# Kernel optimization log

Hardware: AMD Instinct MI355X
Metric: run time of the kernel (lower is better)

## Reference

```python
import jax, jax.numpy as jnp
import numpy as np

N = 100000
E = 1600000
D_IN = 128
D_OUT = 128

def setup_inputs() -> dict:
    key = jax.random.key(0)
    k1, k2, k3, k4, k5, k6 = jax.random.split(key, 6)
    h = jax.random.normal(k1, (N, D_IN), dtype=jnp.float32)
    # norm ~ deg^{-1/2}; use positive uniform values as stand-in
    norm = jax.random.uniform(k2, (N, 1), dtype=jnp.float32, minval=0.05, maxval=1.0)
    src = jax.random.randint(k3, (E,), 0, N, dtype=jnp.int32)
    dst = jax.random.randint(k4, (E,), 0, N, dtype=jnp.int32)
    weight = jax.random.normal(k5, (D_IN, D_OUT), dtype=jnp.float32) * (2.0 / (D_IN + D_OUT)) ** 0.5
    bias = jnp.zeros((D_OUT,), dtype=jnp.float32)
    return {"h": h, "norm": norm, "src": src, "dst": dst, "weight": weight, "bias": bias}

def reference(h, norm, src, dst, weight, bias):
    n_nodes = h.shape[0]
    hw = h @ weight                      # [N, D_out] dense GEMM
    hw = hw * norm                       # pre-aggregation degree scale
    msgs = hw[src]                       # gather: [E, D_out]
    agg = jax.ops.segment_sum(msgs, dst, num_segments=n_nodes)  # scatter-sum
    out = agg * norm + bias              # post-scale + bias
    return out
```

## Files before the change

kernel.cpp:

```cpp
#include <hip/hip_runtime.h>
#include <hip/hip_bf16.h>
#include <hip/hip_cooperative_groups.h>

namespace cg = cooperative_groups;

#define D 128
#define D4 32
#define CHUNK 6400
#define KSLOT 7
#define MAXB 2048
#define NSEG 8
#define SL 4096

typedef __attribute__((ext_vector_type(8))) short bf16x8;
typedef __attribute__((ext_vector_type(8))) unsigned short ushort8;
typedef __attribute__((ext_vector_type(4))) float f32x4;

static __device__ __forceinline__ float bf2f(unsigned short u) {
    return __uint_as_float(((unsigned)u) << 16);
}
static __device__ __forceinline__ unsigned pk2(float x, float y) {
    float2 f; f.x = x; f.y = y;
    __hip_bfloat162 b = __float22bfloat162_rn(f);
    return *(unsigned*)&b;
}

__global__ __launch_bounds__(256) void wcvt_kernel(
    const float* __restrict__ W, unsigned short* __restrict__ Wt)
{
    const int idx = blockIdx.x * 256 + threadIdx.x;
    const float4 w = ((const float4*)W)[idx];
    const int k = idx >> 5;
    const int c = (idx & 31) * 4;
    const unsigned q01 = pk2(w.x, w.y);
    const unsigned q23 = pk2(w.z, w.w);
    Wt[(c + 0) * 128 + k] = (unsigned short)(q01 & 0xFFFFu);
    Wt[(c + 1) * 128 + k] = (unsigned short)(q01 >> 16);
    Wt[(c + 2) * 128 + k] = (unsigned short)(q23 & 0xFFFFu);
    Wt[(c + 3) * 128 + k] = (unsigned short)(q23 >> 16);
}

__global__ __launch_bounds__(512) void gemm_mfma_kernel(
    const float* __restrict__ h, const unsigned short* __restrict__ Wt,
    const float* __restrict__ norm, unsigned short* __restrict__ hwb,
    int n_nodes)
{
    __shared__ unsigned short Bs[128 * 136];

    const int t = threadIdx.x;
    const int row0 = blockIdx.x * 128;

    #pragma unroll
    for (int i = 0; i < 4; ++i) {
        const int idx = t + 512 * i;
        const int c = idx >> 4;
        const int k8 = idx & 15;
        *(ushort8*)&Bs[c * 136 + k8 * 8] = ((const ushort8*)Wt)[idx];
    }
    __syncthreads();

    const int wv = t >> 6;
    const int lane = t & 63;
    const int m = lane & 15;
    const int quad = lane >> 4;

    long gra = row0 + wv * 16 + m;
    if (gra >= n_nodes) gra = n_nodes - 1;
    const float* hrow = h + gra * D;

    f32x4 acc[8];
    #pragma unroll
    for (int nt = 0; nt < 8; ++nt) { f32x4 z = {0.f, 0.f, 0.f, 0.f}; acc[nt] = z; }

    #pragma unroll
    for (int kt = 0; kt < 4; ++kt) {
        const float4 a0 = *(const float4*)(hrow + kt * 32 + quad * 8);
        const float4 a1 = *(const float4*)(hrow + kt * 32 + quad * 8 + 4);
        bf16x8 af;
        unsigned* aw = (unsigned*)&af;
        aw[0] = pk2(a0.x, a0.y);
        aw[1] = pk2(a0.z, a0.w);
        aw[2] = pk2(a1.x, a1.y);
        aw[3] = pk2(a1.z, a1.w);
        #pragma unroll
        for (int nt = 0; nt < 8; ++nt) {
            const bf16x8 bfr = *(const bf16x8*)&Bs[(nt * 16 + m) * 136 + kt * 32 + quad * 8];
            acc[nt] = __builtin_amdgcn_mfma_f32_16x16x32_bf16(af, bfr, acc[nt], 0, 0, 0);
        }
    }

    float nv[4];
    #pragma unroll
    for (int i = 0; i < 4; ++i) {
        const int gr = row0 + wv * 16 + quad * 4 + i;
        nv[i] = (gr < n_nodes) ? norm[gr] : 0.f;
    }

    __syncthreads();
    #pragma unroll
    for (int nt = 0; nt < 8; ++nt) {
        const unsigned q01 = pk2(acc[nt][0] * nv[0], acc[nt][1] * nv[1]);
        const unsigned q23 = pk2(acc[nt][2] * nv[2], acc[nt][3] * nv[3]);
        const int rb = wv * 16 + quad * 4;
        Bs[(rb + 0) * 136 + nt * 16 + m] = (unsigned short)(q01 & 0xFFFFu);
        Bs[(rb + 1) * 136 + nt * 16 + m] = (unsigned short)(q01 >> 16);
        Bs[(rb + 2) * 136 + nt * 16 + m] = (unsigned short)(q23 & 0xFFFFu);
        Bs[(rb + 3) * 136 + nt * 16 + m] = (unsigned short)(q23 >> 16);
    }
    __syncthreads();

    #pragma unroll
    for (int i2 = 0; i2 < 4; ++i2) {
        const int idx = t + 512 * i2;
        const int r = idx >> 4;
        const int c8 = idx & 15;
        const int gr = row0 + r;
        if (gr < n_nodes)
            *(ushort8*)&hwb[(size_t)gr * D + c8 * 8] =
                *(const ushort8*)&Bs[r * 136 + c8 * 8];
    }
}

__global__ __launch_bounds__(1024) void coop_edge_kernel(
    const int* __restrict__ src, const int* __restrict__ dst,
    int* __restrict__ H, int* __restrict__ PS, int* __restrict__ SB,
    int* __restrict__ boff,
    unsigned int* __restrict__ ebuf, int* __restrict__ srcs_g,
    const unsigned short* __restrict__ hwb,
    const float* __restrict__ norm, const float* __restrict__ bias,
    float* __restrict__ out,
    int n_edges, int n_nodes, int EB, int NBUCK)
{
    __shared__ int smem[SL + 192];

    cg::grid_group grid = cg::this_grid();
    const int t = threadIdx.x;
    const int g = blockIdx.x;
    const int gid = g * 1024 + t;
    const int glen = (EB + NSEG - 1) / NSEG;
    const int e0 = g * CHUNK;
    const int e1 = min(e0 + CHUNK, n_edges);

    int ed[KSLOT], es[KSLOT], er[KSLOT];
    {
        int* lbh = smem;
        for (int i = t; i < MAXB; i += 1024) lbh[i] = 0;
        if (g == 0 && t < 32) {
            ushort4 z; z.x = z.y = z.z = z.w = 0;
            ((ushort4*)(hwb + (size_t)n_nodes * D))[t] = z;
        }
        __syncthreads();
        #pragma unroll
        for (int k = 0; k < KSLOT; ++k) {
            const int e = e0 + t + 1024 * k;
            if (e < e1) {
                ed[k] = dst[e];
                es[k] = src[e];
                er[k] = atomicAdd(&lbh[ed[k] >> 6], 1);
            } else { ed[k] = -1; es[k] = 0; er[k] = 0; }
        }
        __syncthreads();
        for (int i = t; i < MAXB; i += 1024) H[(size_t)g * MAXB + i] = lbh[i];
    }
    grid.sync();

    if (gid < NSEG * MAXB) {
        const int seg = gid >> 11;
        const int c = gid & (MAXB - 1);
        const int g0 = seg * glen, g1 = min(g0 + glen, EB);
        int s = 0;
        for (int gg = g0; gg < g1; ++gg) s += H[(size_t)gg * MAXB + c];
        PS[seg * MAXB + c] = s;
    }
    grid.sync();

    if (g == 0) {
        int* tmp = smem;
        const int cA = 2 * t, cB = 2 * t + 1;
        int va = 0, vb = 0;
        #pragma unroll
        for (int sg = 0; sg < NSEG; ++sg) { va += PS[sg * MAXB + cA]; vb += PS[sg * MAXB + cB]; }
        tmp[t] = va + vb;
        __syncthreads();
        for (int ofs = 1; ofs < 1024; ofs <<= 1) {
            const int x = (t >= ofs) ? tmp[t - ofs] : 0;
            __syncthreads();
            tmp[t] += x;
            __syncthreads();
        }
        const int run = tmp[t] - (va + vb);
        boff[cA] = run;
        boff[cB] = run + va;
        if (t == 1023) boff[MAXB] = tmp[1023];
        int sb = run;
        #pragma unroll
        for (int sg = 0; sg < NSEG; ++sg) { SB[sg * MAXB + cA] = sb; sb += PS[sg * MAXB + cA]; }
        sb = run + va;
        #pragma unroll
        for (int sg = 0; sg < NSEG; ++sg) { SB[sg * MAXB + cB] = sb; sb += PS[sg * MAXB + cB]; }
    }
    grid.sync();

    {
        int* lofs = smem;
        const int seg = g / glen;
        const int g0s = seg * glen;
        for (int i = t; i < MAXB; i += 1024) {
            int run = SB[seg * MAXB + i];
            for (int gg = g0s; gg < g; ++gg) run += H[(size_t)gg * MAXB + i];
            lofs[i] = run;
        }
        __syncthreads();
        #pragma unroll
        for (int k = 0; k < KSLOT; ++k) {
            if (ed[k] >= 0)
                ebuf[lofs[ed[k] >> 6] + er[k]] =
                    (unsigned)es[k] | ((unsigned)(ed[k] & 63) << 17);
        }
    }
    grid.sync();

    {
        int* slds = smem;
        int* lcnt = smem + SL;
        int* lcur = smem + SL + 64;
        int* loff = smem + SL + 128;
        const ushort4* hw4 = (const ushort4*)hwb;
        const int grp = t >> 5;
        const int l = t & 31;
        const float4 bs = ((const float4*)bias)[l];

        for (int bkt = g; bkt < NBUCK; bkt += gridDim.x) {
            __syncthreads();
            if (t < 64) lcnt[t] = 0;
            __syncthreads();
            const int w0 = boff[bkt], w1 = boff[bkt + 1];
            const int wlen = w1 - w0;
            const bool uselds = (wlen + 480) <= SL;
            const int gbase = w0 + 448 * bkt;
            const int gn0 = bkt * 64;

            unsigned rc[4];
            if (uselds) {
                #pragma unroll
                for (int k = 0; k < 4; ++k) {
                    const int e = w0 + t + k * 1024;
                    if (e < w1) {
                        rc[k] = ebuf[e];
                        atomicAdd(&lcnt[(rc[k] >> 17) & 63], 1);
                    }
                }
            } else {
                for (int e = w0 + t; e < w1; e += 1024)
                    atomicAdd(&lcnt[(ebuf[e] >> 17) & 63], 1);
            }
            __syncthreads();
            if (t < 64) {
                const int c = lcnt[t];
                const int p = (c + 7) & ~7;
                int x = p;
                #pragma unroll
                for (int ofs = 1; ofs < 64; ofs <<= 1) {
                    const int y = __shfl_up(x, ofs, 64);
                    if (t >= ofs) x += y;
                }
                const int base = x - p;
                lcur[t] = base;
                loff[t] = base;
            }
            __syncthreads();
            if (uselds) {
                #pragma unroll
                for (int k = 0; k < 4; ++k) {
                    const int e = w0 + t + k * 1024;
                    if (e < w1) {
                        const unsigned rec = rc[k];
                        const int loc = (rec >> 17) & 63;
                        const int pos = atomicAdd(&lcur[loc], 1);
                        slds[pos] = (int)(rec & 0x1FFFFu);
                    }
                }
            } else {
                for (int e = w0 + t; e < w1; e += 1024) {
                    const unsigned rec = ebuf[e];
                    const int loc = (rec >> 17) & 63;
                    const int pos = atomicAdd(&lcur[loc], 1);
                    srcs_g[gbase + pos] = (int)(rec & 0x1FFFFu);
                }
            }
            for (int w = t; w < 512; w += 1024) {
                const int ln = w >> 3, k = w & 7;
                const int gn = gn0 + ln;
                if (gn < n_nodes) {
                    const int c = lcnt[ln];
                    const int pad = (8 - (c & 7)) & 7;
                    if (k < pad) {
                        const int pos = loff[ln] + c + k;
                        if (uselds) slds[pos] = n_nodes; else srcs_g[gbase + pos] = n_nodes;
                    }
                }
            }
            __syncthreads();

            #pragma unroll
            for (int nn = 0; nn < 2; ++nn) {
                const int loc = grp * 2 + nn;
                const int gn = gn0 + loc;
                if (gn >= n_nodes) continue;
                const int start = loff[loc];
                const int deg = lcnt[loc];
                const int nb8 = (deg + 7) >> 3;
                float4 acc; acc.x = acc.y = acc.z = acc.w = 0.f;
                int myidx = 0;
                for (int bb = 0; bb < nb8; ++bb) {
                    const int q = bb & 3;
                    if (q == 0) {
                        const int ri = start + bb * 8 + l;
                        myidx = uselds ? slds[ri] : srcs_g[gbase + ri];
                    }
                    ushort4 v[8];
                    #pragma unroll
                    for (int jj = 0; jj < 8; ++jj) {
                        const int s = __shfl(myidx, q * 8 + jj, 32);
                        v[jj] = hw4[(long)s * D4 + l];
                    }
                    #pragma unroll
                    for (int jj = 0; jj < 8; ++jj) {
                        acc.x += bf2f(v[jj].x);
                        acc.y += bf2f(v[jj].y);
                        acc.z += bf2f(v[jj].z);
                        acc.w += bf2f(v[jj].w);
                    }
                }
                const float nv = norm[gn];
                float4 o;
                o.x = acc.x * nv + bs.x;
                o.y = acc.y * nv + bs.y;
                o.z = acc.z * nv + bs.z;
                o.w = acc.w * nv + bs.w;
                ((float4*)out)[(long)gn * D4 + l] = o;
            }
        }
    }
}

__global__ __launch_bounds__(1024) void hist_kernel(
    const int* __restrict__ dst, int* __restrict__ H,
    unsigned short* __restrict__ hwb, int n_edges, int n_nodes)
{
    __shared__ int lbh[MAXB];
    const int t = threadIdx.x;
    const int g = blockIdx.x;
    for (int i = t; i < MAXB; i += 1024) lbh[i] = 0;
    if (g == 0 && t < 32) {
        ushort4 z; z.x = z.y = z.z = z.w = 0;
        ((ushort4*)(hwb + (size_t)n_nodes * D))[t] = z;
    }
    __syncthreads();
    const int e0 = g * CHUNK;
    const int e1 = min(e0 + CHUNK, n_edges);
    for (int e = e0 + t; e < e1; e += 1024) {
        atomicAdd(&lbh[dst[e] >> 6], 1);
    }
    __syncthreads();
    for (int i = t; i < MAXB; i += 1024) {
        H[(size_t)g * MAXB + i] = lbh[i];
    }
}

__global__ __launch_bounds__(256) void chunkscan_local_kernel(
    const int* __restrict__ H, int* __restrict__ CO, int* __restrict__ PS,
    int eb)
{
    const int b = blockIdx.x * 256 + threadIdx.x;
    const int seg = blockIdx.y;
    const int glen = (eb + NSEG - 1) / NSEG;
    const int g0 = seg * glen;
    const int g1 = min(g0 + glen, eb);
    int run = 0;
    for (int g = g0; g < g1; ++g) {
        CO[(size_t)g * MAXB + b] = run;
        run += H[(size_t)g * MAXB + b];
    }
    PS[seg * MAXB + b] = run;
}

__global__ __launch_bounds__(256) void bucket_scan_kernel(
    const int* __restrict__ PS, int* __restrict__ boff, int* __restrict__ SB)
{
    __shared__ int tmp[256];
    const int t = threadIdx.x;
    int v[8];
    int s = 0;
    #pragma unroll
    for (int k = 0; k < 8; ++k) {
        const int i = t * 8 + k;
        int c = 0;
        #pragma unroll
        for (int sg = 0; sg < NSEG; ++sg) c += PS[sg * MAXB + i];
        v[k] = c; s += c;
    }
    tmp[t] = s;
    __syncthreads();
    for (int ofs = 1; ofs < 256; ofs <<= 1) {
        int x = (t >= ofs) ? tmp[t - ofs] : 0;
        __syncthreads();
        tmp[t] += x;
        __syncthreads();
    }
    int run = tmp[t] - s;
    #pragma unroll
    for (int k = 0; k < 8; ++k) {
        const int i = t * 8 + k;
        boff[i] = run;
        int sb = run;
        #pragma unroll
        for (int sg = 0; sg < NSEG; ++sg) {
            SB[sg * MAXB + i] = sb;
            sb += PS[sg * MAXB + i];
        }
        run += v[k];
    }
    if (t == 255) boff[MAXB] = run;
}

__global__ __launch_bounds__(1024) void bscatter_kernel(
    const int* __restrict__ src, const int* __restrict__ dst,
    const int* __restrict__ CO, const int* __restrict__ SB,
    unsigned int* __restrict__ ebuf, int n_edges, int eb)
{
    __shared__ int lbh[MAXB];
    __shared__ int lofs[MAXB];
    const int t = threadIdx.x;
    const int g = blockIdx.x;
    const int glen = (eb + NSEG - 1) / NSEG;
    const int seg = g / glen;
    for (int i = t; i < MAXB; i += 1024) {
        lbh[i] = 0;
        lofs[i] = SB[seg * MAXB + i] + CO[(size_t)g * MAXB + i];
    }
    __syncthreads();
    const int e0 = g * CHUNK;
    const int e1 = min(e0 + CHUNK, n_edges);
    for (int e = e0 + t; e < e1; e += 1024) {
        const int d = dst[e];
        const int bk = d >> 6;
        const int r = atomicAdd(&lbh[bk], 1);
        ebuf[lofs[bk] + r] = (unsigned)src[e] | ((unsigned)(d & 63) << 17);
    }
}

__global__ __launch_bounds__(256) void fillagg_kernel(
    const unsigned int* __restrict__ ebuf, const int* __restrict__ boff,
    int* __restrict__ srcs_g, const unsigned short* __restrict__ hwb,
    const float* __restrict__ norm, const float* __restrict__ bias,
    float* __restrict__ out, int n_nodes)
{
    __shared__ int slds[SL];
    __shared__ int lcnt[64];
    __shared__ int lcur[64];
    __shared__ int loff[64];
    const int t = threadIdx.x;
    const int b = blockIdx.x;
    const int gn0 = b * 64;

    if (t < 64) lcnt[t] = 0;
    __syncthreads();
    const int w0 = boff[b], w1 = boff[b + 1];
    const int wlen = w1 - w0;
    const bool uselds = (wlen + 480) <= SL;
    const int gbase = w0 + 448 * b;

    for (int e = w0 + t; e < w1; e += 256) {
        atomicAdd(&lcnt[(ebuf[e] >> 17) & 63], 1);
    }
    __syncthreads();
    if (t < 64) {
        const int c = lcnt[t];
        const int p = (c + 7) & ~7;
        int x = p;
        #pragma unroll
        for (int ofs = 1; ofs < 64; ofs <<= 1) {
            const int y = __shfl_up(x, ofs, 64);
            if (t >= ofs) x += y;
        }
        const int base = x - p;
        lcur[t] = base;
        loff[t] = base;
    }
    __syncthreads();
    for (int e = w0 + t; e < w1; e += 256) {
        const unsigned rec = ebuf[e];
        const int loc = (rec >> 17) & 63;
        const int pos = atomicAdd(&lcur[loc], 1);
        const int sv = (int)(rec & 0x1FFFFu);
        if (uselds) slds[pos] = sv; else srcs_g[gbase + pos] = sv;
    }
    for (int w = t; w < 512; w += 256) {
        const int ln = w >> 3, k = w & 7;
        const int gn = gn0 + ln;
        if (gn < n_nodes) {
            const int c = lcnt[ln];
            const int pad = (8 - (c & 7)) & 7;
            if (k < pad) {
                const int pos = loff[ln] + c + k;
                if (uselds) slds[pos] = n_nodes; else srcs_g[gbase + pos] = n_nodes;
            }
        }
    }
    __syncthreads();

    const ushort4* hw4 = (const ushort4*)hwb;
    const int grp = t >> 5;
    const int l = t & 31;
    const float4 bs = ((const float4*)bias)[l];
    for (int nn = 0; nn < 8; ++nn) {
        const int loc = grp * 8 + nn;
        const int gn = gn0 + loc;
        if (gn >= n_nodes) continue;
        const int start = loff[loc];
        const int deg = lcnt[loc];
        const int nb8 = (deg + 7) >> 3;
        float4 acc; acc.x = acc.y = acc.z = acc.w = 0.f;
        int myidx = 0;
        for (int bb = 0; bb < nb8; ++bb) {
            const int q = bb & 3;
            if (q == 0) {
                const int ri = start + bb * 8 + l;
                myidx = uselds ? slds[ri] : srcs_g[gbase + ri];
            }
            ushort4 v[8];
            #pragma unroll
            for (int jj = 0; jj < 8; ++jj) {
                const int s = __shfl(myidx, q * 8 + jj, 32);
                v[jj] = hw4[(long)s * D4 + l];
            }
            #pragma unroll
            for (int jj = 0; jj < 8; ++jj) {
                acc.x += bf2f(v[jj].x);
                acc.y += bf2f(v[jj].y);
                acc.z += bf2f(v[jj].z);
                acc.w += bf2f(v[jj].w);
            }
        }
        const float nv = norm[gn];
        float4 o;
        o.x = acc.x * nv + bs.x;
        o.y = acc.y * nv + bs.y;
        o.z = acc.z * nv + bs.z;
        o.w = acc.w * nv + bs.w;
        ((float4*)out)[(long)gn * D4 + l] = o;
    }
}

__global__ __launch_bounds__(256) void scatter_kernel(
    const unsigned short* __restrict__ hwb, const int* __restrict__ src,
    const int* __restrict__ dst, float* __restrict__ out, int n_edges)
{
    const int idx = blockIdx.x * 256 + threadIdx.x;
    if (idx >= n_edges * D4) return;
    const int e = idx >> 5;
    const int g = idx & 31;
    const int s = src[e];
    const int d = dst[e];
    const ushort4 v = ((const ushort4*)hwb)[(long)s * D4 + g];
    float* o = out + (long)d * D + g * 4;
    atomicAdd(o + 0, bf2f(v.x));
    atomicAdd(o + 1, bf2f(v.y));
    atomicAdd(o + 2, bf2f(v.z));
    atomicAdd(o + 3, bf2f(v.w));
}

__global__ __launch_bounds__(256) void finalize_kernel(
    float* __restrict__ out, const float* __restrict__ norm,
    const float* __restrict__ bias, int n_nodes)
{
    const int idx = blockIdx.x * 256 + threadIdx.x;
    if (idx >= n_nodes * D4) return;
    const int n = idx >> 5;
    const int g = idx & 31;
    float4 v = ((float4*)out)[idx];
    const float nv = norm[n];
    const float4 b = ((const float4*)bias)[g];
    v.x = v.x * nv + b.x;
    v.y = v.y * nv + b.y;
    v.z = v.z * nv + b.z;
    v.w = v.w * nv + b.w;
    ((float4*)out)[idx] = v;
}

extern "C" void kernel_launch(void* const* d_in, const int* in_sizes, int n_in,
                              void* d_out, int out_size, void* d_ws, size_t ws_size,
                              hipStream_t stream) {
    const float* h    = (const float*)d_in[0];
    const float* norm = (const float*)d_in[1];
    const int*   src  = (const int*)d_in[2];
    const int*   dst  = (const int*)d_in[3];
    const float* W    = (const float*)d_in[4];
    const float* bias = (const float*)d_in[5];
    float* out = (float*)d_out;

    const int n_nodes = in_sizes[1];
    const int n_edges = in_sizes[2];

    const int NBUCK = (n_nodes + 63) >> 6;
    const int EB    = (n_edges + CHUNK - 1) / CHUNK;
    const int srcs_len = n_edges + 448 * NBUCK + 64;

    size_t p = 0;
    auto take = [&](size_t bytes) {
        size_t cur = p;
        p += (bytes + 255) & ~(size_t)255;
        return cur;
    };
    const size_t hwb_off  = take(((size_t)n_nodes + 1) * D * sizeof(unsigned short));
    const size_t wt_off   = take((size_t)D * D * sizeof(unsigned short));
    const size_t srcs_off = take((size_t)srcs_len * sizeof(int));
    const size_t ebuf_off = take((size_t)n_edges * sizeof(unsigned int));
    const size_t boff_off = take((MAXB + 1) * sizeof(int));
    const size_t H_off    = take((size_t)EB * MAXB * sizeof(int));
    const size_t PS_off   = take((size_t)NSEG * MAXB * sizeof(int));
    const size_t SB_off   = take((size_t)NSEG * MAXB * sizeof(int));
    const size_t CO_off   = take((size_t)EB * MAXB * sizeof(int));
    const size_t needed = p;

    char* ws = (char*)d_ws;
    unsigned short* hwb = (unsigned short*)(ws + hwb_off);
    unsigned short* Wt  = (unsigned short*)(ws + wt_off);

    wcvt_kernel<<<16, 256, 0, stream>>>(W, Wt);
    gemm_mfma_kernel<<<(n_nodes + 127) / 128, 512, 0, stream>>>(h, Wt, norm, hwb, n_nodes);

    static int s_max_coop_blocks = -1;
    if (s_max_coop_blocks < 0) {
        int nb = 0;
        if (hipOccupancyMaxActiveBlocksPerMultiprocessor(&nb, coop_edge_kernel, 1024, 0)
            != hipSuccess) nb = 0;
        int dev = 0;
        hipGetDevice(&dev);
        int ncu = 0;
        if (hipDeviceGetAttribute(&ncu, hipDeviceAttributeMultiprocessorCount, dev)
            != hipSuccess) ncu = 0;
        s_max_coop_blocks = nb * ncu;
    }

    const bool ws_ok = (ws_size >= needed) && (NBUCK <= MAXB) && (n_nodes <= 131072);
    const bool coop_ok = ws_ok && EB >= 16 && EB <= 512 && EB <= s_max_coop_blocks;

    if (coop_ok) {
        int* srcs  = (int*)(ws + srcs_off);
        unsigned int* ebuf = (unsigned int*)(ws + ebuf_off);
        int* boff  = (int*)(ws + boff_off);
        int* H     = (int*)(ws + H_off);
        int* PS    = (int*)(ws + PS_off);
        int* SBp   = (int*)(ws + SB_off);

        int ne = n_edges, nn = n_nodes, eb = EB, nbk = NBUCK;
        void* args[] = {
            (void*)&src, (void*)&dst, (void*)&H, (void*)&PS, (void*)&SBp,
            (void*)&boff, (void*)&ebuf, (void*)&srcs, (void*)&hwb,
            (void*)&norm, (void*)&bias, (void*)&out,
            (void*)&ne, (void*)&nn, (void*)&eb, (void*)&nbk
        };
        hipLaunchCooperativeKernel((void*)coop_edge_kernel, dim3(EB), dim3(1024),
                                   args, 0, stream);
    } else if (ws_ok && EB <= 1024) {
        int* srcs  = (int*)(ws + srcs_off);
        unsigned int* ebuf = (unsigned int*)(ws + ebuf_off);
        int* boff  = (int*)(ws + boff_off);
        int* H     = (int*)(ws + H_off);
        int* PS    = (int*)(ws + PS_off);
        int* SBp   = (int*)(ws + SB_off);
        int* CO    = (int*)(ws + CO_off);

        hist_kernel<<<EB, 1024, 0, stream>>>(dst, H, hwb, n_edges, n_nodes);
        chunkscan_local_kernel<<<dim3(MAXB / 256, NSEG), 256, 0, stream>>>(H, CO, PS, EB);
        bucket_scan_kernel<<<1, 256, 0, stream>>>(PS, boff, SBp);
        bscatter_kernel<<<EB, 1024, 0, stream>>>(src, dst, CO, SBp, ebuf, n_edges, EB);
        fillagg_kernel<<<NBUCK, 256, 0, stream>>>(ebuf, boff, srcs, hwb, norm, bias,
                                                  out, n_nodes);
    } else {
        hipMemsetAsync(d_out, 0, (size_t)out_size * sizeof(float), stream);
        const int work = n_edges * D4;
        scatter_kernel<<<(work + 255) / 256, 256, 0, stream>>>(hwb, src, dst, out, n_edges);
        const int work2 = n_nodes * D4;
        finalize_kernel<<<(work2 + 255) / 256, 256, 0, stream>>>(out, norm, bias, n_nodes);
    }
}
```

Measured before the change: 229.3 us.

## Replace grid syncs in bucket scan with global atomics and last-block ticket

Drops the per-block histogram array, the segmented partial-sum passes and three grid-wide barriers from the cooperative edge kernel. Blocks now add their local bucket counts atomically into a global counter array, and the last block to arrive (chosen by ticket) scans it while the other blocks spin on a flag. Each block then claims its output range per bucket with an atomicAdd on a cursor array. This removes barrier and scan latency, but makes edge order within a bucket nondeterministic, which can change float summation order. It also adds a memset launch and global atomic contention on about 2048 counters.

```diff
diff --git a/kernel.cpp b/kernel.cpp
--- a/kernel.cpp
+++ b/kernel.cpp
@@ -123,8 +123,8 @@
 
 __global__ __launch_bounds__(1024) void coop_edge_kernel(
     const int* __restrict__ src, const int* __restrict__ dst,
-    int* __restrict__ H, int* __restrict__ PS, int* __restrict__ SB,
-    int* __restrict__ boff,
+    int* __restrict__ bcnt, int* __restrict__ ctrl,
+    int* __restrict__ boff, int* __restrict__ bcur,
     unsigned int* __restrict__ ebuf, int* __restrict__ srcs_g,
     const unsigned short* __restrict__ hwb,
     const float* __restrict__ norm, const float* __restrict__ bias,
@@ -132,83 +132,86 @@
     int n_edges, int n_nodes, int EB, int NBUCK)
 {
     __shared__ int smem[SL + 192];
+    __shared__ int amLast;
+    int* lbh = smem;
+    int* aux = smem + MAXB;
 
     cg::grid_group grid = cg::this_grid();
     const int t = threadIdx.x;
     const int g = blockIdx.x;
-    const int gid = g * 1024 + t;
-    const int glen = (EB + NSEG - 1) / NSEG;
     const int e0 = g * CHUNK;
     const int e1 = min(e0 + CHUNK, n_edges);
 
     int ed[KSLOT], es[KSLOT], er[KSLOT];
-    {
-        int* lbh = smem;
-        for (int i = t; i < MAXB; i += 1024) lbh[i] = 0;
-        if (g == 0 && t < 32) {
-            ushort4 z; z.x = z.y = z.z = z.w = 0;
-            ((ushort4*)(hwb + (size_t)n_nodes * D))[t] = z;
-        }
-        __syncthreads();
-        #pragma unroll
-        for (int k = 0; k < KSLOT; ++k) {
-            const int e = e0 + t + 1024 * k;
-            if (e < e1) {
-                ed[k] = dst[e];
-                es[k] = src[e];
-                er[k] = atomicAdd(&lbh[ed[k] >> 6], 1);
-            } else { ed[k] = -1; es[k] = 0; er[k] = 0; }
-        }
-        __syncthreads();
-        for (int i = t; i < MAXB; i += 1024) H[(size_t)g * MAXB + i] = lbh[i];
-    }
-    grid.sync();
-
-    if (gid < NSEG * MAXB) {
-        const int seg = gid >> 11;
-        const int c = gid & (MAXB - 1);
-        const int g0 = seg * glen, g1 = min(g0 + glen, EB);
-        int s = 0;
-        for (int gg = g0; gg < g1; ++gg) s += H[(size_t)gg * MAXB + c];
-        PS[seg * MAXB + c] = s;
-    }
-    grid.sync();
-
-    if (g == 0) {
-        int* tmp = smem;
+    for (int i = t; i < MAXB; i += 1024) lbh[i] = 0;
+    if (g == 0 && t < 32) {
+        ushort4 z; z.x = z.y = z.z = z.w = 0;
+        ((ushort4*)(hwb + (size_t)n_nodes * D))[t] = z;
+    }
+    __syncthreads();
+    #pragma unroll
+    for (int k = 0; k < KSLOT; ++k) {
+        const int e = e0 + t + 1024 * k;
+        if (e < e1) {
+            ed[k] = dst[e];
+            es[k] = src[e];
+            er[k] = atomicAdd(&lbh[ed[k] >> 6], 1);
+        } else { ed[k] = -1; es[k] = 0; er[k] = 0; }
+    }
+    __syncthreads();
+    for (int i = t; i < MAXB; i += 1024) {
+        const int c = lbh[i];
+        if (c) atomicAdd(&bcnt[i], c);
+    }
+
+    __threadfence();
+    __syncthreads();
+    if (t == 0) {
+        const int ticket = __hip_atomic_fetch_add(&ctrl[0], 1,
+                              __ATOMIC_ACQ_REL, __HIP_MEMORY_SCOPE_AGENT);
+        amLast = (ticket == EB - 1) ? 1 : 0;
+    }
+    __syncthreads();
+    if (amLast) {
         const int cA = 2 * t, cB = 2 * t + 1;
-        int va = 0, vb = 0;
-        #pragma unroll
-        for (int sg = 0; sg < NSEG; ++sg) { va += PS[sg * MAXB + cA]; vb += PS[sg * MAXB + cB]; }
-        tmp[t] = va + vb;
+        const int va = __hip_atomic_load(&bcnt[cA], __ATOMIC_RELAXED,
+                                         __HIP_MEMORY_SCOPE_AGENT);
+        const int vb = __hip_atomic_load(&bcnt[cB], __ATOMIC_RELAXED,
+                                         __HIP_MEMORY_SCOPE_AGENT);
+        aux[t] = va + vb;
         __syncthreads();
         for (int ofs = 1; ofs < 1024; ofs <<= 1) {
-            const int x = (t >= ofs) ? tmp[t - ofs] : 0;
+            const int x = (t >= ofs) ? aux[t - ofs] : 0;
             __syncthreads();
-            tmp[t] += x;
+            aux[t] += x;
             __syncthreads();
         }
-        const int run = tmp[t] - (va + vb);
-        boff[cA] = run;
-        boff[cB] = run + va;
-        if (t == 1023) boff[MAXB] = tmp[1023];
-        int sb = run;
-        #pragma unroll
-        for (int sg = 0; sg < NSEG; ++sg) { SB[sg * MAXB + cA] = sb; sb += PS[sg * MAXB + cA]; }
-        sb = run + va;
-        #pragma unroll
-        for (int sg = 0; sg < NSEG; ++sg) { SB[sg * MAXB + cB] = sb; sb += PS[sg * MAXB + cB]; }
-    }
-    grid.sync();
+        const int run = aux[t] - (va + vb);
+        __hip_atomic_store(&boff[cA], run, __ATOMIC_RELAXED, __HIP_MEMORY_SCOPE_AGENT);
+        __hip_atomic_store(&boff[cB], run + va, __ATOMIC_RELAXED, __HIP_MEMORY_SCOPE_AGENT);
+        __hip_atomic_store(&bcur[cA], run, __ATOMIC_RELAXED, __HIP_MEMORY_SCOPE_AGENT);
+        __hip_atomic_store(&bcur[cB], run + va, __ATOMIC_RELAXED, __HIP_MEMORY_SCOPE_AGENT);
+        if (t == 1023)
+            __hip_atomic_store(&boff[MAXB], aux[1023], __ATOMIC_RELAXED,
+                               __HIP_MEMORY_SCOPE_AGENT);
+        __syncthreads();
+        if (t == 0)
+            __hip_atomic_store(&ctrl[1], 1, __ATOMIC_RELEASE,
+                               __HIP_MEMORY_SCOPE_AGENT);
+    } else {
+        if (t == 0) {
+            while (__hip_atomic_load(&ctrl[1], __ATOMIC_ACQUIRE,
+                                     __HIP_MEMORY_SCOPE_AGENT) == 0)
+                __builtin_amdgcn_s_sleep(2);
+        }
+        __syncthreads();
+    }
 
     {
-        int* lofs = smem;
-        const int seg = g / glen;
-        const int g0s = seg * glen;
+        int* lofs = aux;
         for (int i = t; i < MAXB; i += 1024) {
-            int run = SB[seg * MAXB + i];
-            for (int gg = g0s; gg < g; ++gg) run += H[(size_t)gg * MAXB + i];
-            lofs[i] = run;
+            const int c = lbh[i];
+            lofs[i] = c ? atomicAdd(&bcur[i], c) : 0;
         }
         __syncthreads();
         #pragma unroll
@@ -618,6 +621,8 @@
     const size_t srcs_off = take((size_t)srcs_len * sizeof(int));
     const size_t ebuf_off = take((size_t)n_edges * sizeof(unsigned int));
     const size_t boff_off = take((MAXB + 1) * sizeof(int));
+    const size_t bcur_off = take(MAXB * sizeof(int));
+    const size_t zr_off   = take((MAXB + 2) * sizeof(int));
     const size_t H_off    = take((size_t)EB * MAXB * sizeof(int));
     const size_t PS_off   = take((size_t)NSEG * MAXB * sizeof(int));
     const size_t SB_off   = take((size_t)NSEG * MAXB * sizeof(int));
@@ -651,14 +656,16 @@
         int* srcs  = (int*)(ws + srcs_off);
         unsigned int* ebuf = (unsigned int*)(ws + ebuf_off);
         int* boff  = (int*)(ws + boff_off);
-        int* H     = (int*)(ws + H_off);
-        int* PS    = (int*)(ws + PS_off);
-        int* SBp   = (int*)(ws + SB_off);
+        int* bcur  = (int*)(ws + bcur_off);
+        int* bcnt  = (int*)(ws + zr_off);
+        int* ctrl  = bcnt + MAXB;
+
+        hipMemsetAsync(ws + zr_off, 0, (MAXB + 2) * sizeof(int), stream);
 
         int ne = n_edges, nn = n_nodes, eb = EB, nbk = NBUCK;
         void* args[] = {
-            (void*)&src, (void*)&dst, (void*)&H, (void*)&PS, (void*)&SBp,
-            (void*)&boff, (void*)&ebuf, (void*)&srcs, (void*)&hwb,
+            (void*)&src, (void*)&dst, (void*)&bcnt, (void*)&ctrl,
+            (void*)&boff, (void*)&bcur, (void*)&ebuf, (void*)&srcs, (void*)&hwb,
             (void*)&norm, (void*)&bias, (void*)&out,
             (void*)&ne, (void*)&nn, (void*)&eb, (void*)&nbk
         };
```

Result: no change. 229.1 us (-0.1%).
